# Optimization experiments

Hardware: AMD Instinct MI355X
Metric: run time of the kernel (lower is better)

## Reference

```python
import jax, jax.numpy as jnp
import numpy as np

N_NODES = 50000
N_EDGES = 800000
D = 128          # embedding_dim
G = 3            # group_size
K = 4            # window_size
ALPHA = -0.5
WEIGHTS = (1.0, 1.0, 7.81, 45.28)
EPS = 1e-12      # torch F.normalize clamp_min


def _striped_projection(key):
    """Striped sparse random projection, densified (matches torch coalesce+to_dense)."""
    num_groups = D // G  # 42; columns 126..127 remain zero, as in the original
    k_off, k_sign = jax.random.split(key)
    row_idx = jnp.repeat(jnp.arange(N_NODES), num_groups)
    base = jnp.tile(jnp.arange(0, num_groups * G, G), N_NODES)
    off = jax.random.randint(k_off, (N_NODES * num_groups,), 0, G)
    col_idx = base + off
    scale = float(np.sqrt(G))  # 1/sqrt(density), density = 1/g
    vals = (jax.random.randint(k_sign, (N_NODES * num_groups,), 0, 2).astype(jnp.float32) * 2.0 - 1.0) * scale
    return jnp.zeros((N_NODES, D), jnp.float32).at[row_idx, col_idx].add(vals)


def setup_inputs() -> dict:
    key = jax.random.key(0)
    k1, k2, k3 = jax.random.split(key, 3)
    edge_row = jax.random.randint(k1, (N_EDGES,), 0, N_NODES)
    edge_col = jax.random.randint(k2, (N_EDGES,), 0, N_NODES)
    edge_val = jnp.ones((N_EDGES,), jnp.float32)
    R = _striped_projection(k3)
    return {"edge_row": edge_row, "edge_col": edge_col, "edge_val": edge_val, "R": R}


def reference(edge_row, edge_col, edge_val, R):
    N = R.shape[0]
    # degrees = row sums of sparse adjacency; zeros -> 1
    deg = jax.ops.segment_sum(edge_val, edge_row, num_segments=N)
    deg = jnp.where(deg == 0, 1.0, deg)
    # initial degree scaling: N_curr = R * deg**alpha
    x = R * (deg ** ALPHA)[:, None]
    inv_deg = (1.0 / deg)[:, None]
    acc = jnp.zeros_like(R)
    for i in range(K):
        # SpMM: out[r] = sum_{e: row[e]==r} val[e] * x[col[e]]
        x = jax.ops.segment_sum(edge_val[:, None] * x[edge_col], edge_row, num_segments=N)
        x = x * inv_deg  # transition-matrix ('trans') scaling
        nrm = jnp.maximum(jnp.sqrt(jnp.sum(x * x, axis=1, keepdims=True)), EPS)
        acc = acc + (x / nrm) * WEIGHTS[i]
    mean = acc.mean(axis=0)
    std = jnp.std(acc, axis=0, ddof=1)  # torch .std() is unbiased
    std = jnp.where(std == 0, 1.0, std)
    return (acc - mean) / std
```

## Files before the change

kernel.cpp:

```cpp
#include <hip/hip_runtime.h>
#include <math.h>

#define NN 50000
#define NE 800000
#define DD 128
#define NBKT 196
#define BCAP 5120
#define CHUNK 2048
#define NCHUNK ((NE + CHUNK - 1) / CHUNK)
#define CS1_NBLK 1024
#define CS_ROWS 49

static __device__ __forceinline__ float blo(unsigned int p) { return __uint_as_float(p << 16); }
static __device__ __forceinline__ float bhi(unsigned int p) { return __uint_as_float(p & 0xffff0000u); }
static __device__ __forceinline__ unsigned int pack2bf(float a, float b) {
    unsigned int ua = __float_as_uint(a);
    unsigned int ub = __float_as_uint(b);
    ua = ua + 0x7FFFu + ((ua >> 16) & 1u);
    ub = ub + 0x7FFFu + ((ub >> 16) & 1u);
    return (ua >> 16) | (ub & 0xffff0000u);
}

static __global__ __launch_bounds__(256) void bin_kernel(
    const int* __restrict__ erow, const int* __restrict__ ecol, const float* __restrict__ eval_,
    int* __restrict__ bucket_cursor, uint2* __restrict__ binned) {
    __shared__ uint2 sorted[CHUNK];
    __shared__ unsigned short sbin[CHUNK];
    __shared__ int hist[NBKT];
    __shared__ int bstart[NBKT];
    __shared__ int bcur[NBKT];
    __shared__ int gbase[NBKT];
    __shared__ int tmp[256];

    int t = threadIdx.x;
    int cbase = blockIdx.x * CHUNK;
    int cn = NE - cbase; if (cn > CHUNK) cn = CHUNK;

    for (int i = t; i < NBKT; i += 256) hist[i] = 0;
    __syncthreads();

    unsigned int rc[8]; unsigned int vv[8]; int bb[8];
    int nloc = 0;
    for (int i = t; i < cn; i += 256) {
        int g = cbase + i;
        int r = erow[g];
        int c = ecol[g];
        float v = eval_[g];
        rc[nloc] = (unsigned)r | ((unsigned)c << 16);
        vv[nloc] = __float_as_uint(v);
        int b = r >> 8;
        bb[nloc] = b;
        atomicAdd(&hist[b], 1);
        ++nloc;
    }
    __syncthreads();

    int hv = (t < NBKT) ? hist[t] : 0;
    tmp[t] = hv;
    __syncthreads();
    for (int off = 1; off < 256; off <<= 1) {
        int u = (t >= off) ? tmp[t - off] : 0;
        __syncthreads();
        tmp[t] += u;
        __syncthreads();
    }
    if (t < NBKT) {
        int ex = tmp[t] - hv;
        bstart[t] = ex;
        bcur[t] = ex;
        gbase[t] = atomicAdd(&bucket_cursor[t], hv);
    }
    __syncthreads();

    for (int k = 0; k < nloc; ++k) {
        int pos = atomicAdd(&bcur[bb[k]], 1);
        sorted[pos] = make_uint2(rc[k], vv[k]);
        sbin[pos] = (unsigned short)bb[k];
    }
    __syncthreads();

    for (int i = t; i < cn; i += 256) {
        int b = sbin[i];
        binned[(size_t)b * BCAP + gbase[b] + (i - bstart[b])] = sorted[i];
    }
}

static __global__ void bucket_scan_kernel(const int* __restrict__ bucket_cursor,
                                          int* __restrict__ bucket_base) {
    __shared__ int tmp[256];
    int t = threadIdx.x;
    int v = (t < NBKT) ? bucket_cursor[t] : 0;
    tmp[t] = v;
    __syncthreads();
    for (int off = 1; off < 256; off <<= 1) {
        int u = (t >= off) ? tmp[t - off] : 0;
        __syncthreads();
        tmp[t] += u;
        __syncthreads();
    }
    if (t < NBKT) bucket_base[t] = tmp[t] - v;
}

static __global__ __launch_bounds__(256) void sort_kernel(
    const uint2* __restrict__ binned, const int* __restrict__ bucket_cursor,
    const int* __restrict__ bucket_base, uint2* __restrict__ csr, int* __restrict__ row_start) {
    __shared__ uint2 buf[BCAP];
    __shared__ int hist[256];
    __shared__ int rcur[256];
    int b = blockIdx.x;
    int t = threadIdx.x;
    int cnt = bucket_cursor[b];
    int gb = bucket_base[b];
    int lo = b << 8;

    hist[t] = 0;
    __syncthreads();
    for (int i = t; i < cnt; i += 256) {
        uint2 e = binned[(size_t)b * BCAP + i];
        buf[i] = e;
        atomicAdd(&hist[(e.x & 0xFFFFu) - lo], 1);
    }
    __syncthreads();
    int hv = hist[t];
    rcur[t] = hv;
    __syncthreads();
    for (int off = 1; off < 256; off <<= 1) {
        int u = (t >= off) ? rcur[t - off] : 0;
        __syncthreads();
        rcur[t] += u;
        __syncthreads();
    }
    int excl = rcur[t] - hv;
    int r = lo + t;
    if (r < NN) row_start[r] = gb + excl;
    if (b == NBKT - 1 && t == 255) row_start[NN] = gb + cnt;
    rcur[t] = excl;
    __syncthreads();
    for (int i = t; i < cnt; i += 256) {
        uint2 e = buf[i];
        int rr = (int)(e.x & 0xFFFFu) - lo;
        int pos = atomicAdd(&rcur[rr], 1);
        csr[(size_t)gb + pos] = make_uint2(e.x >> 16, e.y);
    }
}

static __global__ void deg_from_csr_kernel(const int* __restrict__ row_start,
                                           const uint2* __restrict__ csr,
                                           float* __restrict__ deg, int n) {
    int r = blockIdx.x * blockDim.x + threadIdx.x;
    if (r < n) {
        int s = row_start[r], e = row_start[r + 1];
        float sum = 0.0f;
        for (int j = s; j < e; ++j) sum += __uint_as_float(csr[j].y);
        deg[r] = (sum == 0.0f) ? 1.0f : sum;
    }
}

static __global__ void init_x_kernel(const float* __restrict__ R, const float* __restrict__ deg,
                                     uint4* __restrict__ xq, int nquads) {
    int i = blockIdx.x * blockDim.x + threadIdx.x;
    if (i < nquads) {
        float d = deg[i >> 4];
        float sc = rsqrtf(d);
        const float4* R4 = (const float4*)R;
        float4 f0 = R4[i * 2];
        float4 f1 = R4[i * 2 + 1];
        xq[i] = make_uint4(pack2bf(f0.x * sc, f0.y * sc), pack2bf(f0.z * sc, f0.w * sc),
                           pack2bf(f1.x * sc, f1.y * sc), pack2bf(f1.z * sc, f1.w * sc));
    }
}

static __global__ __launch_bounds__(256) void spmm_fused_kernel(
    const int* __restrict__ row_start, const uint2* __restrict__ csr,
    const uint4* __restrict__ x4, const float* __restrict__ deg,
    uint4* __restrict__ x_next4, float* __restrict__ s_out, float weight) {
    int wave = threadIdx.x >> 6;
    int lane = threadIdx.x & 63;
    int quarter = lane >> 4;
    int sub = lane & 15;
    int row = blockIdx.x * 4 + wave;
    int s = row_start[row];
    int e = row_start[row + 1];

    float a0 = 0.f, a1 = 0.f, a2 = 0.f, a3 = 0.f, a4 = 0.f, a5 = 0.f, a6 = 0.f, a7 = 0.f;
    for (int base = s; base < e; base += 64) {
        int j = base + lane;
        int cl = 0;
        float vl = 0.0f;
        if (j < e) { uint2 t2 = csr[j]; cl = (int)t2.x; vl = __uint_as_float(t2.y); }
        int cnt = e - base; if (cnt > 64) cnt = 64;
        int k = 0;
        for (; k + 8 <= cnt; k += 8) {
            int ca = __shfl(cl, k + quarter);
            int cb = __shfl(cl, k + 4 + quarter);
            float va = __shfl(vl, k + quarter);
            float vb = __shfl(vl, k + 4 + quarter);
            uint4 pa = x4[(size_t)ca * 16 + sub];
            uint4 pb = x4[(size_t)cb * 16 + sub];
            a0 += va * blo(pa.x); a1 += va * bhi(pa.x); a2 += va * blo(pa.y); a3 += va * bhi(pa.y);
            a4 += va * blo(pa.z); a5 += va * bhi(pa.z); a6 += va * blo(pa.w); a7 += va * bhi(pa.w);
            a0 += vb * blo(pb.x); a1 += vb * bhi(pb.x); a2 += vb * blo(pb.y); a3 += vb * bhi(pb.y);
            a4 += vb * blo(pb.z); a5 += vb * bhi(pb.z); a6 += vb * blo(pb.w); a7 += vb * bhi(pb.w);
        }
        for (; k < cnt; k += 4) {
            int kk = k + quarter;
            int c = __shfl(cl, kk);
            float v = __shfl(vl, kk);
            uint4 p = x4[(size_t)c * 16 + sub];
            a0 += v * blo(p.x); a1 += v * bhi(p.x); a2 += v * blo(p.y); a3 += v * bhi(p.y);
            a4 += v * blo(p.z); a5 += v * bhi(p.z); a6 += v * blo(p.w); a7 += v * bhi(p.w);
        }
    }
    a0 += __shfl_xor(a0, 16); a1 += __shfl_xor(a1, 16); a2 += __shfl_xor(a2, 16); a3 += __shfl_xor(a3, 16);
    a4 += __shfl_xor(a4, 16); a5 += __shfl_xor(a5, 16); a6 += __shfl_xor(a6, 16); a7 += __shfl_xor(a7, 16);
    a0 += __shfl_xor(a0, 32); a1 += __shfl_xor(a1, 32); a2 += __shfl_xor(a2, 32); a3 += __shfl_xor(a3, 32);
    a4 += __shfl_xor(a4, 32); a5 += __shfl_xor(a5, 32); a6 += __shfl_xor(a6, 32); a7 += __shfl_xor(a7, 32);

    float id = 1.0f / deg[row];
    a0 *= id; a1 *= id; a2 *= id; a3 *= id; a4 *= id; a5 *= id; a6 *= id; a7 *= id;

    float ss = a0 * a0 + a1 * a1 + a2 * a2 + a3 * a3 + a4 * a4 + a5 * a5 + a6 * a6 + a7 * a7;
#pragma unroll
    for (int m = 1; m <= 8; m <<= 1) ss += __shfl_xor(ss, m);
    float nrm = fmaxf(sqrtf(ss), 1e-12f);

    if (lane < 16) {
        x_next4[(size_t)row * 16 + sub] = make_uint4(pack2bf(a0, a1), pack2bf(a2, a3),
                                                     pack2bf(a4, a5), pack2bf(a6, a7));
    }
    if (lane == 0) s_out[row] = weight / nrm;
}

static __global__ __launch_bounds__(256) void combine_stats_kernel(
    const uint4* __restrict__ x1, const uint4* __restrict__ x2,
    const uint4* __restrict__ x3, const uint4* __restrict__ x4,
    const float* __restrict__ s1, const float* __restrict__ s2,
    const float* __restrict__ s3, const float* __restrict__ s4,
    float* __restrict__ out, double* __restrict__ psum, double* __restrict__ psumsq) {
    __shared__ double shs[256 * 8];
    __shared__ double shq[256 * 8];
    int t = threadIdx.x;
    int sub = t & 15;
    int ro = t >> 4;
    int rbeg = blockIdx.x * CS_ROWS;
    int rend = rbeg + CS_ROWS; if (rend > NN) rend = NN;

    double ls[8], lq[8];
#pragma unroll
    for (int j = 0; j < 8; ++j) { ls[j] = 0.0; lq[j] = 0.0; }

    float4* out4 = (float4*)out;
    for (int r = rbeg + ro; r < rend; r += 16) {
        float w1 = s1[r], w2 = s2[r], w3 = s3[r], w4 = s4[r];
        size_t xi = (size_t)r * 16 + sub;
        uint4 q1 = x1[xi], q2 = x2[xi], q3 = x3[xi], q4 = x4[xi];
        float v[8];
        v[0] = w1 * blo(q1.x) + w2 * blo(q2.x) + w3 * blo(q3.x) + w4 * blo(q4.x);
        v[1] = w1 * bhi(q1.x) + w2 * bhi(q2.x) + w3 * bhi(q3.x) + w4 * bhi(q4.x);
        v[2] = w1 * blo(q1.y) + w2 * blo(q2.y) + w3 * blo(q3.y) + w4 * blo(q4.y);
        v[3] = w1 * bhi(q1.y) + w2 * bhi(q2.y) + w3 * bhi(q3.y) + w4 * bhi(q4.y);
        v[4] = w1 * blo(q1.z) + w2 * blo(q2.z) + w3 * blo(q3.z) + w4 * blo(q4.z);
        v[5] = w1 * bhi(q1.z) + w2 * bhi(q2.z) + w3 * bhi(q3.z) + w4 * bhi(q4.z);
        v[6] = w1 * blo(q1.w) + w2 * blo(q2.w) + w3 * blo(q3.w) + w4 * blo(q4.w);
        v[7] = w1 * bhi(q1.w) + w2 * bhi(q2.w) + w3 * bhi(q3.w) + w4 * bhi(q4.w);
        out4[(size_t)r * 32 + sub * 2]     = make_float4(v[0], v[1], v[2], v[3]);
        out4[(size_t)r * 32 + sub * 2 + 1] = make_float4(v[4], v[5], v[6], v[7]);
#pragma unroll
        for (int j = 0; j < 8; ++j) { ls[j] += (double)v[j]; lq[j] += (double)v[j] * (double)v[j]; }
    }
#pragma unroll
    for (int j = 0; j < 8; ++j) { shs[t * 8 + j] = ls[j]; shq[t * 8 + j] = lq[j]; }
    __syncthreads();
    if (t < DD) {
        int cs = t >> 3, cj = t & 7;
        double s = 0.0, q = 0.0;
        for (int g = 0; g < 16; ++g) {
            int src = (g * 16 + cs) * 8 + cj;
            s += shs[src];
            q += shq[src];
        }
        psum[(size_t)blockIdx.x * DD + t] = s;
        psumsq[(size_t)blockIdx.x * DD + t] = q;
    }
}

static __global__ __launch_bounds__(256) void colstats_fold_kernel(
    const double* __restrict__ psum, const double* __restrict__ psumsq,
    float* __restrict__ mean, float* __restrict__ invstd) {
    __shared__ double ss[256], qq[256];
    int c = blockIdx.x;
    int t = threadIdx.x;
    double s = 0.0, q = 0.0;
    for (int b = t; b < CS1_NBLK; b += 256) {
        s += psum[(size_t)b * DD + c];
        q += psumsq[(size_t)b * DD + c];
    }
    ss[t] = s; qq[t] = q;
    __syncthreads();
    for (int off = 128; off > 0; off >>= 1) {
        if (t < off) { ss[t] += ss[t + off]; qq[t] += qq[t + off]; }
        __syncthreads();
    }
    if (t == 0) {
        double m = ss[0] / (double)NN;
        double var = (qq[0] - (double)NN * m * m) / (double)(NN - 1);
        if (var < 0.0) var = 0.0;
        double sd = sqrt(var);
        if (sd == 0.0) sd = 1.0;
        mean[c] = (float)m;
        invstd[c] = (float)(1.0 / sd);
    }
}

static __global__ void normalize_kernel(float* __restrict__ out, const float* __restrict__ mean,
                                        const float* __restrict__ invstd, int total) {
    int i = blockIdx.x * blockDim.x + threadIdx.x;
    if (i < total) {
        int c = i & 127;
        out[i] = (out[i] - mean[c]) * invstd[c];
    }
}

extern "C" void kernel_launch(void* const* d_in, const int* in_sizes, int n_in,
                              void* d_out, int out_size, void* d_ws, size_t ws_size,
                              hipStream_t stream) {
    const int* erow = (const int*)d_in[0];
    const int* ecol = (const int*)d_in[1];
    const float* eval_ = (const float*)d_in[2];
    const float* R = (const float*)d_in[3];
    float* out = (float*)d_out;

    char* ws = (char*)d_ws;
    size_t off = 0;
    auto alloc = [&](size_t bytes) -> char* {
        char* p = ws + off;
        off += (bytes + 255) & ~(size_t)255;
        return p;
    };
    float* deg          = (float*)alloc(NN * sizeof(float));
    int* bucket_cursor  = (int*)alloc(NBKT * sizeof(int));
    int* bucket_base    = (int*)alloc(NBKT * sizeof(int));
    int* row_start      = (int*)alloc((NN + 1) * sizeof(int));
    uint2* binned       = (uint2*)alloc((size_t)NBKT * BCAP * sizeof(uint2));
    uint2* csr          = (uint2*)alloc((size_t)NE * sizeof(uint2));
    uint4* x0           = (uint4*)alloc((size_t)NN * 16 * sizeof(uint4));
    uint4* x1           = (uint4*)alloc((size_t)NN * 16 * sizeof(uint4));
    uint4* x2           = (uint4*)alloc((size_t)NN * 16 * sizeof(uint4));
    uint4* x3           = (uint4*)alloc((size_t)NN * 16 * sizeof(uint4));
    uint4* x4           = (uint4*)alloc((size_t)NN * 16 * sizeof(uint4));
    float* s1           = (float*)alloc(NN * sizeof(float));
    float* s2           = (float*)alloc(NN * sizeof(float));
    float* s3           = (float*)alloc(NN * sizeof(float));
    float* s4           = (float*)alloc(NN * sizeof(float));
    double* psum        = (double*)alloc((size_t)CS1_NBLK * DD * sizeof(double));
    double* psumsq      = (double*)alloc((size_t)CS1_NBLK * DD * sizeof(double));
    float* meanbuf      = (float*)alloc(DD * sizeof(float));
    float* invstdb      = (float*)alloc(DD * sizeof(float));

    hipMemsetAsync(bucket_cursor, 0, NBKT * sizeof(int), stream);

    const int total = NN * DD;
    const int nquads = total / 8;

    bin_kernel<<<NCHUNK, 256, 0, stream>>>(erow, ecol, eval_, bucket_cursor, binned);
    bucket_scan_kernel<<<1, 256, 0, stream>>>(bucket_cursor, bucket_base);
    sort_kernel<<<NBKT, 256, 0, stream>>>(binned, bucket_cursor, bucket_base, csr, row_start);

    deg_from_csr_kernel<<<(NN + 255) / 256, 256, 0, stream>>>(row_start, csr, deg, NN);
    init_x_kernel<<<(nquads + 255) / 256, 256, 0, stream>>>(R, deg, x0, nquads);

    spmm_fused_kernel<<<NN / 4, 256, 0, stream>>>(row_start, csr, x0, deg, x1, s1, 1.0f);
    spmm_fused_kernel<<<NN / 4, 256, 0, stream>>>(row_start, csr, x1, deg, x2, s2, 1.0f);
    spmm_fused_kernel<<<NN / 4, 256, 0, stream>>>(row_start, csr, x2, deg, x3, s3, 7.81f);
    spmm_fused_kernel<<<NN / 4, 256, 0, stream>>>(row_start, csr, x3, deg, x4, s4, 45.28f);

    combine_stats_kernel<<<CS1_NBLK, 256, 0, stream>>>(x1, x2, x3, x4, s1, s2, s3, s4,
                                                       out, psum, psumsq);
    colstats_fold_kernel<<<DD, 256, 0, stream>>>(psum, psumsq, meanbuf, invstdb);
    normalize_kernel<<<(total + 255) / 256, 256, 0, stream>>>(out, meanbuf, invstdb, total);
}
```

Baseline: 273.7 us.

## Map one row per quarter-wave in SpMM, fuse degree into sort, recompute output in final pass

```diff
diff --git a/kernel.cpp b/kernel.cpp
--- a/kernel.cpp
+++ b/kernel.cpp
@@ -103,10 +103,12 @@
 
 static __global__ __launch_bounds__(256) void sort_kernel(
     const uint2* __restrict__ binned, const int* __restrict__ bucket_cursor,
-    const int* __restrict__ bucket_base, uint2* __restrict__ csr, int* __restrict__ row_start) {
+    const int* __restrict__ bucket_base, uint2* __restrict__ csr, int* __restrict__ row_start,
+    float* __restrict__ deg) {
     __shared__ uint2 buf[BCAP];
     __shared__ int hist[256];
     __shared__ int rcur[256];
+    __shared__ float fdeg[256];
     int b = blockIdx.x;
     int t = threadIdx.x;
     int cnt = bucket_cursor[b];
@@ -114,11 +116,14 @@
     int lo = b << 8;
 
     hist[t] = 0;
+    fdeg[t] = 0.0f;
     __syncthreads();
     for (int i = t; i < cnt; i += 256) {
         uint2 e = binned[(size_t)b * BCAP + i];
         buf[i] = e;
-        atomicAdd(&hist[(e.x & 0xFFFFu) - lo], 1);
+        int rr = (int)(e.x & 0xFFFFu) - lo;
+        atomicAdd(&hist[rr], 1);
+        atomicAdd(&fdeg[rr], __uint_as_float(e.y));
     }
     __syncthreads();
     int hv = hist[t];
@@ -132,7 +137,11 @@
     }
     int excl = rcur[t] - hv;
     int r = lo + t;
-    if (r < NN) row_start[r] = gb + excl;
+    if (r < NN) {
+        row_start[r] = gb + excl;
+        float d = fdeg[t];
+        deg[r] = (d == 0.0f) ? 1.0f : d;
+    }
     if (b == NBKT - 1 && t == 255) row_start[NN] = gb + cnt;
     rcur[t] = excl;
     __syncthreads();
@@ -141,18 +150,6 @@
         int rr = (int)(e.x & 0xFFFFu) - lo;
         int pos = atomicAdd(&rcur[rr], 1);
         csr[(size_t)gb + pos] = make_uint2(e.x >> 16, e.y);
-    }
-}
-
-static __global__ void deg_from_csr_kernel(const int* __restrict__ row_start,
-                                           const uint2* __restrict__ csr,
-                                           float* __restrict__ deg, int n) {
-    int r = blockIdx.x * blockDim.x + threadIdx.x;
-    if (r < n) {
-        int s = row_start[r], e = row_start[r + 1];
-        float sum = 0.0f;
-        for (int j = s; j < e; ++j) sum += __uint_as_float(csr[j].y);
-        deg[r] = (sum == 0.0f) ? 1.0f : sum;
     }
 }
 
@@ -178,43 +175,41 @@
     int lane = threadIdx.x & 63;
     int quarter = lane >> 4;
     int sub = lane & 15;
-    int row = blockIdx.x * 4 + wave;
+    int row = blockIdx.x * 16 + wave * 4 + quarter;
     int s = row_start[row];
     int e = row_start[row + 1];
 
     float a0 = 0.f, a1 = 0.f, a2 = 0.f, a3 = 0.f, a4 = 0.f, a5 = 0.f, a6 = 0.f, a7 = 0.f;
-    for (int base = s; base < e; base += 64) {
-        int j = base + lane;
+    for (int base = s; base < e; base += 16) {
+        int j = base + sub;
         int cl = 0;
         float vl = 0.0f;
         if (j < e) { uint2 t2 = csr[j]; cl = (int)t2.x; vl = __uint_as_float(t2.y); }
-        int cnt = e - base; if (cnt > 64) cnt = 64;
-        int k = 0;
-        for (; k + 8 <= cnt; k += 8) {
-            int ca = __shfl(cl, k + quarter);
-            int cb = __shfl(cl, k + 4 + quarter);
-            float va = __shfl(vl, k + quarter);
-            float vb = __shfl(vl, k + 4 + quarter);
-            uint4 pa = x4[(size_t)ca * 16 + sub];
-            uint4 pb = x4[(size_t)cb * 16 + sub];
-            a0 += va * blo(pa.x); a1 += va * bhi(pa.x); a2 += va * blo(pa.y); a3 += va * bhi(pa.y);
-            a4 += va * blo(pa.z); a5 += va * bhi(pa.z); a6 += va * blo(pa.w); a7 += va * bhi(pa.w);
-            a0 += vb * blo(pb.x); a1 += vb * bhi(pb.x); a2 += vb * blo(pb.y); a3 += vb * bhi(pb.y);
-            a4 += vb * blo(pb.z); a5 += vb * bhi(pb.z); a6 += vb * blo(pb.w); a7 += vb * bhi(pb.w);
+        int cnt = e - base; if (cnt > 16) cnt = 16;
+        for (int k = 0; k < cnt; k += 4) {
+            int l0 = quarter * 16 + k;
+            int c0 = __shfl(cl, l0);
+            int c1 = __shfl(cl, l0 + 1);
+            int c2 = __shfl(cl, l0 + 2);
+            int c3 = __shfl(cl, l0 + 3);
+            float v0 = __shfl(vl, l0);
+            float v1 = __shfl(vl, l0 + 1);
+            float v2 = __shfl(vl, l0 + 2);
+            float v3 = __shfl(vl, l0 + 3);
+            uint4 p0 = x4[(size_t)c0 * 16 + sub];
+            uint4 p1 = x4[(size_t)c1 * 16 + sub];
+            uint4 p2 = x4[(size_t)c2 * 16 + sub];
+            uint4 p3 = x4[(size_t)c3 * 16 + sub];
+            a0 += v0 * blo(p0.x); a1 += v0 * bhi(p0.x); a2 += v0 * blo(p0.y); a3 += v0 * bhi(p0.y);
+            a4 += v0 * blo(p0.z); a5 += v0 * bhi(p0.z); a6 += v0 * blo(p0.w); a7 += v0 * bhi(p0.w);
+            a0 += v1 * blo(p1.x); a1 += v1 * bhi(p1.x); a2 += v1 * blo(p1.y); a3 += v1 * bhi(p1.y);
+            a4 += v1 * blo(p1.z); a5 += v1 * bhi(p1.z); a6 += v1 * blo(p1.w); a7 += v1 * bhi(p1.w);
+            a0 += v2 * blo(p2.x); a1 += v2 * bhi(p2.x); a2 += v2 * blo(p2.y); a3 += v2 * bhi(p2.y);
+            a4 += v2 * blo(p2.z); a5 += v2 * bhi(p2.z); a6 += v2 * blo(p2.w); a7 += v2 * bhi(p2.w);
+            a0 += v3 * blo(p3.x); a1 += v3 * bhi(p3.x); a2 += v3 * blo(p3.y); a3 += v3 * bhi(p3.y);
+            a4 += v3 * blo(p3.z); a5 += v3 * bhi(p3.z); a6 += v3 * blo(p3.w); a7 += v3 * bhi(p3.w);
         }
-        for (; k < cnt; k += 4) {
-            int kk = k + quarter;
-            int c = __shfl(cl, kk);
-            float v = __shfl(vl, kk);
-            uint4 p = x4[(size_t)c * 16 + sub];
-            a0 += v * blo(p.x); a1 += v * bhi(p.x); a2 += v * blo(p.y); a3 += v * bhi(p.y);
-            a4 += v * blo(p.z); a5 += v * bhi(p.z); a6 += v * blo(p.w); a7 += v * bhi(p.w);
-        }
-    }
-    a0 += __shfl_xor(a0, 16); a1 += __shfl_xor(a1, 16); a2 += __shfl_xor(a2, 16); a3 += __shfl_xor(a3, 16);
-    a4 += __shfl_xor(a4, 16); a5 += __shfl_xor(a5, 16); a6 += __shfl_xor(a6, 16); a7 += __shfl_xor(a7, 16);
-    a0 += __shfl_xor(a0, 32); a1 += __shfl_xor(a1, 32); a2 += __shfl_xor(a2, 32); a3 += __shfl_xor(a3, 32);
-    a4 += __shfl_xor(a4, 32); a5 += __shfl_xor(a5, 32); a6 += __shfl_xor(a6, 32); a7 += __shfl_xor(a7, 32);
+    }
 
     float id = 1.0f / deg[row];
     a0 *= id; a1 *= id; a2 *= id; a3 *= id; a4 *= id; a5 *= id; a6 *= id; a7 *= id;
@@ -224,19 +219,17 @@
     for (int m = 1; m <= 8; m <<= 1) ss += __shfl_xor(ss, m);
     float nrm = fmaxf(sqrtf(ss), 1e-12f);
 
-    if (lane < 16) {
-        x_next4[(size_t)row * 16 + sub] = make_uint4(pack2bf(a0, a1), pack2bf(a2, a3),
-                                                     pack2bf(a4, a5), pack2bf(a6, a7));
-    }
-    if (lane == 0) s_out[row] = weight / nrm;
-}
-
-static __global__ __launch_bounds__(256) void combine_stats_kernel(
+    x_next4[(size_t)row * 16 + sub] = make_uint4(pack2bf(a0, a1), pack2bf(a2, a3),
+                                                 pack2bf(a4, a5), pack2bf(a6, a7));
+    if (sub == 0) s_out[row] = weight / nrm;
+}
+
+static __global__ __launch_bounds__(256) void stats_kernel(
     const uint4* __restrict__ x1, const uint4* __restrict__ x2,
     const uint4* __restrict__ x3, const uint4* __restrict__ x4,
     const float* __restrict__ s1, const float* __restrict__ s2,
     const float* __restrict__ s3, const float* __restrict__ s4,
-    float* __restrict__ out, double* __restrict__ psum, double* __restrict__ psumsq) {
+    double* __restrict__ psum, double* __restrict__ psumsq) {
     __shared__ double shs[256 * 8];
     __shared__ double shq[256 * 8];
     int t = threadIdx.x;
@@ -249,7 +242,6 @@
 #pragma unroll
     for (int j = 0; j < 8; ++j) { ls[j] = 0.0; lq[j] = 0.0; }
 
-    float4* out4 = (float4*)out;
     for (int r = rbeg + ro; r < rend; r += 16) {
         float w1 = s1[r], w2 = s2[r], w3 = s3[r], w4 = s4[r];
         size_t xi = (size_t)r * 16 + sub;
@@ -263,8 +255,6 @@
         v[5] = w1 * bhi(q1.z) + w2 * bhi(q2.z) + w3 * bhi(q3.z) + w4 * bhi(q4.z);
         v[6] = w1 * blo(q1.w) + w2 * blo(q2.w) + w3 * blo(q3.w) + w4 * blo(q4.w);
         v[7] = w1 * bhi(q1.w) + w2 * bhi(q2.w) + w3 * bhi(q3.w) + w4 * bhi(q4.w);
-        out4[(size_t)r * 32 + sub * 2]     = make_float4(v[0], v[1], v[2], v[3]);
-        out4[(size_t)r * 32 + sub * 2 + 1] = make_float4(v[4], v[5], v[6], v[7]);
 #pragma unroll
         for (int j = 0; j < 8; ++j) { ls[j] += (double)v[j]; lq[j] += (double)v[j] * (double)v[j]; }
     }
@@ -312,13 +302,36 @@
     }
 }
 
-static __global__ void normalize_kernel(float* __restrict__ out, const float* __restrict__ mean,
-                                        const float* __restrict__ invstd, int total) {
+static __global__ __launch_bounds__(256) void final_kernel(
+    const uint4* __restrict__ x1, const uint4* __restrict__ x2,
+    const uint4* __restrict__ x3, const uint4* __restrict__ x4,
+    const float* __restrict__ s1, const float* __restrict__ s2,
+    const float* __restrict__ s3, const float* __restrict__ s4,
+    const float* __restrict__ mean, const float* __restrict__ invstd,
+    float* __restrict__ out) {
     int i = blockIdx.x * blockDim.x + threadIdx.x;
-    if (i < total) {
-        int c = i & 127;
-        out[i] = (out[i] - mean[c]) * invstd[c];
-    }
+    int r = i >> 4;
+    int sub = i & 15;
+    float w1 = s1[r], w2 = s2[r], w3 = s3[r], w4 = s4[r];
+    uint4 q1 = x1[i], q2 = x2[i], q3 = x3[i], q4 = x4[i];
+    float v[8];
+    v[0] = w1 * blo(q1.x) + w2 * blo(q2.x) + w3 * blo(q3.x) + w4 * blo(q4.x);
+    v[1] = w1 * bhi(q1.x) + w2 * bhi(q2.x) + w3 * bhi(q3.x) + w4 * bhi(q4.x);
+    v[2] = w1 * blo(q1.y) + w2 * blo(q2.y) + w3 * blo(q3.y) + w4 * blo(q4.y);
+    v[3] = w1 * bhi(q1.y) + w2 * bhi(q2.y) + w3 * bhi(q3.y) + w4 * bhi(q4.y);
+    v[4] = w1 * blo(q1.z) + w2 * blo(q2.z) + w3 * blo(q3.z) + w4 * blo(q4.z);
+    v[5] = w1 * bhi(q1.z) + w2 * bhi(q2.z) + w3 * bhi(q3.z) + w4 * bhi(q4.z);
+    v[6] = w1 * blo(q1.w) + w2 * blo(q2.w) + w3 * blo(q3.w) + w4 * blo(q4.w);
+    v[7] = w1 * bhi(q1.w) + w2 * bhi(q2.w) + w3 * bhi(q3.w) + w4 * bhi(q4.w);
+    const float4* m4 = (const float4*)mean;
+    const float4* is4 = (const float4*)invstd;
+    float4 m0 = m4[sub * 2], m1 = m4[sub * 2 + 1];
+    float4 i0 = is4[sub * 2], i1 = is4[sub * 2 + 1];
+    float4* out4 = (float4*)out;
+    out4[(size_t)i * 2]     = make_float4((v[0] - m0.x) * i0.x, (v[1] - m0.y) * i0.y,
+                                          (v[2] - m0.z) * i0.z, (v[3] - m0.w) * i0.w);
+    out4[(size_t)i * 2 + 1] = make_float4((v[4] - m1.x) * i1.x, (v[5] - m1.y) * i1.y,
+                                          (v[6] - m1.z) * i1.z, (v[7] - m1.w) * i1.w);
 }
 
 extern "C" void kernel_launch(void* const* d_in, const int* in_sizes, int n_in,
@@ -364,18 +377,17 @@
 
     bin_kernel<<<NCHUNK, 256, 0, stream>>>(erow, ecol, eval_, bucket_cursor, binned);
     bucket_scan_kernel<<<1, 256, 0, stream>>>(bucket_cursor, bucket_base);
-    sort_kernel<<<NBKT, 256, 0, stream>>>(binned, bucket_cursor, bucket_base, csr, row_start);
-
-    deg_from_csr_kernel<<<(NN + 255) / 256, 256, 0, stream>>>(row_start, csr, deg, NN);
+    sort_kernel<<<NBKT, 256, 0, stream>>>(binned, bucket_cursor, bucket_base, csr, row_start, deg);
+
     init_x_kernel<<<(nquads + 255) / 256, 256, 0, stream>>>(R, deg, x0, nquads);
 
-    spmm_fused_kernel<<<NN / 4, 256, 0, stream>>>(row_start, csr, x0, deg, x1, s1, 1.0f);
-    spmm_fused_kernel<<<NN / 4, 256, 0, stream>>>(row_start, csr, x1, deg, x2, s2, 1.0f);
-    spmm_fused_kernel<<<NN / 4, 256, 0, stream>>>(row_start, csr, x2, deg, x3, s3, 7.81f);
-    spmm_fused_kernel<<<NN / 4, 256, 0, stream>>>(row_start, csr, x3, deg, x4, s4, 45.28f);
-
-    combine_stats_kernel<<<CS1_NBLK, 256, 0, stream>>>(x1, x2, x3, x4, s1, s2, s3, s4,
-                                                       out, psum, psumsq);
+    spmm_fused_kernel<<<NN / 16, 256, 0, stream>>>(row_start, csr, x0, deg, x1, s1, 1.0f);
+    spmm_fused_kernel<<<NN / 16, 256, 0, stream>>>(row_start, csr, x1, deg, x2, s2, 1.0f);
+    spmm_fused_kernel<<<NN / 16, 256, 0, stream>>>(row_start, csr, x2, deg, x3, s3, 7.81f);
+    spmm_fused_kernel<<<NN / 16, 256, 0, stream>>>(row_start, csr, x3, deg, x4, s4, 45.28f);
+
+    stats_kernel<<<CS1_NBLK, 256, 0, stream>>>(x1, x2, x3, x4, s1, s2, s3, s4, psum, psumsq);
     colstats_fold_kernel<<<DD, 256, 0, stream>>>(psum, psumsq, meanbuf, invstdb);
-    normalize_kernel<<<(total + 255) / 256, 256, 0, stream>>>(out, meanbuf, invstdb, total);
-}
+    final_kernel<<<NN * 16 / 256, 256, 0, stream>>>(x1, x2, x3, x4, s1, s2, s3, s4,
+                                                    meanbuf, invstdb, out);
+}
```

Measured after the change: 253.4 us. 1.08x faster.
